# Optimization experiments

Hardware: AMD Instinct MI355X
Metric: run time of the kernel (lower is better)

The kernel has to match this reference:

```python
import jax, jax.numpy as jnp
import numpy as np

N_EMBD = 1024
N_HEAD = 16
LN_EPS = 1e-5


def layernorm(x, w, eps=LN_EPS):
    mu = jnp.mean(x, axis=-1, keepdims=True)
    var = jnp.mean(jnp.square(x - mu), axis=-1, keepdims=True)
    return (x - mu) * jax.lax.rsqrt(var + eps) * w


def setup_inputs() -> dict:
    key = jax.random.key(0)
    ks = jax.random.split(key, 6)
    B, T, C, F = 4, 2048, N_EMBD, 4 * N_EMBD
    s = 0.02
    return {
        "x": jax.random.normal(ks[0], (B, T, C), jnp.float32),
        "ln1_w": jnp.ones((C,), jnp.float32),
        "w_attn": jax.random.normal(ks[1], (C, 3 * C), jnp.float32) * s,
        "w_proj": jax.random.normal(ks[2], (C, C), jnp.float32) * s,
        "ln2_w": jnp.ones((C,), jnp.float32),
        "w_fc1": jax.random.normal(ks[3], (C, F), jnp.float32) * s,
        "b_fc1": jnp.zeros((F,), jnp.float32),
        "w_fc2": jax.random.normal(ks[4], (F, C), jnp.float32) * s,
        "b_fc2": jnp.zeros((C,), jnp.float32),
    }


def reference(x, ln1_w, w_attn, w_proj, ln2_w, w_fc1, b_fc1, w_fc2, b_fc2):
    B, T, C = x.shape
    H = N_HEAD
    D = C // H
    # --- attention sub-block (dropout = 0, eval mode) ---
    h = layernorm(x, ln1_w)
    qkv = h @ w_attn  # [B, T, 3C]
    q, k, v = jnp.split(qkv, 3, axis=-1)
    q = q.reshape(B, T, H, D)
    k = k.reshape(B, T, H, D)
    v = v.reshape(B, T, H, D)
    scale = 1.0 / np.sqrt(D).astype(np.float32)
    att = jnp.einsum("bqhd,bkhd->bhqk", q, k) * scale  # [B, H, T, T]
    causal = jnp.tril(jnp.ones((T, T), bool))
    att = jnp.where(causal, att, -jnp.inf)
    att = jax.nn.softmax(att, axis=-1)
    y = jnp.einsum("bhqk,bkhd->bqhd", att, v).reshape(B, T, C)
    x = x + y @ w_proj
    # --- MLP sub-block ---
    h = layernorm(x, ln2_w)
    h = jax.nn.relu(h @ w_fc1 + b_fc1)
    x = x + (h @ w_fc2 + b_fc2)
    return x
```

## Files before the change

### kernel.cpp

```cpp
#include <hip/hip_runtime.h>
#include <cstdint>


#define CDIM 1024
#define TSEQ 2048
#define NBATCH 4
#define NHEAD 16
#define HDIM 64
#define FDIM 4096

typedef unsigned short u16;
typedef __attribute__((ext_vector_type(8))) short s16x8;
typedef __attribute__((ext_vector_type(4))) float f32x4;

__device__ __forceinline__ u16 f2bu(float f) {
    uint32_t u = __builtin_bit_cast(uint32_t, f);
    uint32_t r = (u + 0x7FFFu + ((u >> 16) & 1u)) >> 16;
    return (u16)r;
}

__device__ __forceinline__ uint32_t cvtpk(float lo, float hi) {
    uint32_t r;
    asm("v_cvt_pk_bf16_f32 %0, %1, %2" : "=v"(r) : "v"(lo), "v"(hi));
    return r;
}

typedef __attribute__((address_space(3))) unsigned int lds_u32;
typedef __attribute__((address_space(1))) const unsigned int glb_u32;
__device__ __forceinline__ void gload_lds16(const void* g, void* l) {
    __builtin_amdgcn_global_load_lds((glb_u32*)g, (lds_u32*)l, 16, 0, 0);
}

__global__ __launch_bounds__(256) void twb_k(const float* __restrict__ in,
                                             u16* __restrict__ out, int K, int N) {
    __shared__ float tile[32][33];
    int n0 = blockIdx.x * 32, k0 = blockIdx.y * 32;
    int tx = threadIdx.x & 31, ty = threadIdx.x >> 5;
#pragma unroll
    for (int i = 0; i < 32; i += 8)
        tile[ty + i][tx] = in[(size_t)(k0 + ty + i) * N + n0 + tx];
    __syncthreads();
#pragma unroll
    for (int i = 0; i < 32; i += 8)
        out[(size_t)(n0 + ty + i) * K + k0 + tx] = f2bu(tile[tx][ty + i]);
}

__global__ __launch_bounds__(256) void ln_k(const float* __restrict__ x,
                                            const float* __restrict__ w,
                                            u16* __restrict__ out) {
    int row = blockIdx.x;
    int t = threadIdx.x;
    const float4* xr = (const float4*)(x + (size_t)row * CDIM);
    float4 v = xr[t];
    float s = v.x + v.y + v.z + v.w;
    float sq = v.x * v.x + v.y * v.y + v.z * v.z + v.w * v.w;
#pragma unroll
    for (int o = 32; o > 0; o >>= 1) { s += __shfl_xor(s, o); sq += __shfl_xor(sq, o); }
    __shared__ float ps[4], pq[4];
    int wid = t >> 6, lane = t & 63;
    if (lane == 0) { ps[wid] = s; pq[wid] = sq; }
    __syncthreads();
    s = ps[0] + ps[1] + ps[2] + ps[3];
    sq = pq[0] + pq[1] + pq[2] + pq[3];
    float mu = s * (1.0f / CDIM);
    float var = sq * (1.0f / CDIM) - mu * mu;
    float rstd = rsqrtf(var + 1e-5f);
    float4 wv = ((const float4*)w)[t];
    union { u16 h[4]; uint2 u; } pk;
    pk.h[0] = f2bu((v.x - mu) * rstd * wv.x);
    pk.h[1] = f2bu((v.y - mu) * rstd * wv.y);
    pk.h[2] = f2bu((v.z - mu) * rstd * wv.z);
    pk.h[3] = f2bu((v.w - mu) * rstd * wv.w);
    ((uint2*)(out + (size_t)row * CDIM))[t] = pk.u;
}

template <int EPI>
__global__ __launch_bounds__(256) void gemm_bt(const u16* __restrict__ A,
                                               const u16* __restrict__ Bt,
                                               void* __restrict__ Cout,
                                               u16* __restrict__ Vout,
                                               const float* __restrict__ bias,
                                               const float* __restrict__ res,
                                               int M, int N, int K) {
    __shared__ u16 Al[128 * 32];
    __shared__ u16 Bl[128 * 32];
    int tid = threadIdx.x;
    int lane = tid & 63, wid = tid >> 6;
    int wr = wid >> 1, wc = wid & 1;
    int lr = lane & 15, lk = lane >> 4;
    int m0 = blockIdx.y * 128, n0 = blockIdx.x * 128;

    f32x4 acc[4][4];
#pragma unroll
    for (int i = 0; i < 4; ++i)
#pragma unroll
        for (int j = 0; j < 4; ++j) acc[i][j] = (f32x4){0.f, 0.f, 0.f, 0.f};

    for (int k0 = 0; k0 < K; k0 += 32) {
        __syncthreads();
#pragma unroll
        for (int i = 0; i < 2; ++i) {
            int cb = (wid * 2 + i) * 64;
            int c = cb + lane;
            int r = c >> 2, kc = c & 3;
            gload_lds16(A + (size_t)(m0 + r) * K + k0 + kc * 8, Al + cb * 8);
            gload_lds16(Bt + (size_t)(n0 + r) * K + k0 + kc * 8, Bl + cb * 8);
        }
        __syncthreads();
        s16x8 af[4], bfr[4];
#pragma unroll
        for (int mi = 0; mi < 4; ++mi)
            af[mi] = *(const s16x8*)(Al + (wr * 64 + mi * 16 + lr) * 32 + lk * 8);
#pragma unroll
        for (int ni = 0; ni < 4; ++ni)
            bfr[ni] = *(const s16x8*)(Bl + (wc * 64 + ni * 16 + lr) * 32 + lk * 8);
#pragma unroll
        for (int mi = 0; mi < 4; ++mi)
#pragma unroll
            for (int ni = 0; ni < 4; ++ni)
                acc[mi][ni] = __builtin_amdgcn_mfma_f32_16x16x32_bf16(
                    af[mi], bfr[ni], acc[mi][ni], 0, 0, 0);
    }

#pragma unroll
    for (int mi = 0; mi < 4; ++mi) {
#pragma unroll
        for (int ni = 0; ni < 4; ++ni) {
            int col = n0 + wc * 64 + ni * 16 + lr;
#pragma unroll
            for (int r = 0; r < 4; ++r) {
                int row = m0 + wr * 64 + mi * 16 + lk * 4 + r;
                float v = acc[mi][ni][r];
                size_t idx = (size_t)row * N + col;
                if constexpr (EPI == 0) {
                    if (col < 2048) {
                        ((u16*)Cout)[idx] = f2bu(v);
                    } else {
                        int bb = row >> 11, tt = row & 2047, cc = col - 2048;
                        Vout[((size_t)(bb * 16 + (cc >> 6)) * 64 + (cc & 63)) * 2048 + tt] = f2bu(v);
                    }
                } else if constexpr (EPI == 1) {
                    ((float*)Cout)[idx] = res[idx] + v;
                } else if constexpr (EPI == 2) {
                    ((u16*)Cout)[idx] = f2bu(fmaxf(v + bias[col], 0.f));
                } else {
                    ((float*)Cout)[idx] = res[idx] + v + bias[col];
                }
            }
        }
    }
}

__global__ __launch_bounds__(256) void attn_k(const u16* __restrict__ qkv,
                                              const u16* __restrict__ vT,
                                              u16* __restrict__ y) {
    int pidx = blockIdx.x;
    int bh = blockIdx.y;
    int b = bh >> 4, h = bh & 15;
    int tid = threadIdx.x, lane = tid & 63, wid = tid >> 6;
    int lr = lane & 15, lk = lane >> 4;

    __shared__ u16 Kl[2][8192];
    __shared__ u16 Vl[2][8192];

    const u16* qkp = qkv + (size_t)(b * TSEQ) * 3072 + h * HDIM;
    const u16* kkp = qkp + CDIM;
    const u16* vtp = vT + (size_t)bh * HDIM * TSEQ;

    auto STAGE = [&](int buf, int kv0) {
#pragma unroll
        for (int c = 0; c < 4; ++c) {
            int s = c * 256 + wid * 64 + lane;
            int kr = s >> 3, kc = s & 7;
            int gkc = kc ^ (kr & 7);
            gload_lds16(kkp + (size_t)(kv0 + kr) * 3072 + gkc * 8,
                        &Kl[buf][(size_t)(c * 256 + wid * 64) * 8]);
            int vd = s >> 4, vc = s & 15;
            int gvc = (vc & 8) | ((vc ^ vd) & 7);
            gload_lds16(vtp + (size_t)vd * TSEQ + kv0 + gvc * 8,
                        &Vl[buf][(size_t)(c * 256 + wid * 64) * 8]);
        }
    };

    auto qtile = [&](int qt) {
        int qbase = qt * 128 + wid * 32;
        int qend = qbase + 31;
        s16x8 qf[2][2];
#pragma unroll
        for (int qs = 0; qs < 2; ++qs)
#pragma unroll
            for (int db = 0; db < 2; ++db)
                qf[qs][db] = *(const s16x8*)(qkp +
                    (size_t)(qbase + qs * 16 + lr) * 3072 + db * 32 + lk * 8);
        f32x4 acc[2][4];
#pragma unroll
        for (int qs = 0; qs < 2; ++qs)
#pragma unroll
            for (int ds = 0; ds < 4; ++ds) acc[qs][ds] = (f32x4){0.f, 0.f, 0.f, 0.f};
        float mrun[2] = {-1e30f, -1e30f};
        float lrun[2] = {0.f, 0.f};

        int nt = qt + 1;
        STAGE(0, 0);
        for (int t = 0; t < nt; ++t) {
            int cur = t & 1;
            int kv0 = t * 128;
            if (t + 1 < nt) {
                STAGE(cur ^ 1, (t + 1) * 128);
                asm volatile("s_waitcnt vmcnt(8)" ::: "memory");
            } else {
                asm volatile("s_waitcnt vmcnt(0)" ::: "memory");
            }
            __builtin_amdgcn_s_barrier();
            asm volatile("" ::: "memory");

            const u16* Kb = &Kl[cur][0];
            const u16* Vb = &Vl[cur][0];

            f32x4 st[8][2];
#pragma unroll
            for (int ks = 0; ks < 8; ++ks)
#pragma unroll
                for (int qs = 0; qs < 2; ++qs)
                    st[ks][qs] = (f32x4){-1e30f, -1e30f, -1e30f, -1e30f};
            __builtin_amdgcn_s_setprio(1);
#pragma unroll
            for (int ks = 0; ks < 8; ++ks) {
                if (kv0 + ks * 16 <= qend) {
                    s16x8 kf0 = *(const s16x8*)(Kb + (ks * 16 + lr) * 64 + ((lk ^ (lr & 7)) * 8));
                    s16x8 kf1 = *(const s16x8*)(Kb + (ks * 16 + lr) * 64 + (((4 + lk) ^ (lr & 7)) * 8));
#pragma unroll
                    for (int qs = 0; qs < 2; ++qs) {
                        f32x4 z = (f32x4){0.f, 0.f, 0.f, 0.f};
                        z = __builtin_amdgcn_mfma_f32_16x16x32_bf16(kf0, qf[qs][0], z, 0, 0, 0);
                        st[ks][qs] = __builtin_amdgcn_mfma_f32_16x16x32_bf16(kf1, qf[qs][1], z, 0, 0, 0);
                    }
                }
            }
            __builtin_amdgcn_s_setprio(0);

            if (kv0 + 127 > qbase) {
#pragma unroll
                for (int ks = 0; ks < 8; ++ks)
#pragma unroll
                    for (int qs = 0; qs < 2; ++qs)
#pragma unroll
                        for (int r = 0; r < 4; ++r) {
                            int k = kv0 + ks * 16 + lk * 4 + r;
                            int q = qbase + qs * 16 + lr;
                            if (k > q) st[ks][qs][r] = -1e30f;
                        }
            }

            uint32_t w[2][8][2];
#pragma unroll
            for (int qs = 0; qs < 2; ++qs) {
                float pmax = -1e30f;
#pragma unroll
                for (int ks = 0; ks < 8; ++ks) {
                    float a = fmaxf(fmaxf(st[ks][qs][0], st[ks][qs][1]),
                                    fmaxf(st[ks][qs][2], st[ks][qs][3]));
                    pmax = fmaxf(pmax, a);
                }
                pmax = fmaxf(pmax, __shfl_xor(pmax, 16));
                pmax = fmaxf(pmax, __shfl_xor(pmax, 32));
                float mnew = fmaxf(mrun[qs], pmax);
                float scale = __expf((mrun[qs] - mnew) * 0.125f);
                mrun[qs] = mnew;
                float psum = 0.f;
#pragma unroll
                for (int ks = 0; ks < 8; ++ks) {
#pragma unroll
                    for (int r = 0; r < 4; ++r) {
                        float pv = __expf((st[ks][qs][r] - mnew) * 0.125f);
                        st[ks][qs][r] = pv;
                        psum += pv;
                    }
                    w[qs][ks][0] = cvtpk(st[ks][qs][0], st[ks][qs][1]);
                    w[qs][ks][1] = cvtpk(st[ks][qs][2], st[ks][qs][3]);
                }
                psum += __shfl_xor(psum, 16);
                psum += __shfl_xor(psum, 32);
                lrun[qs] = lrun[qs] * scale + psum;
#pragma unroll
                for (int ds = 0; ds < 4; ++ds)
#pragma unroll
                    for (int r = 0; r < 4; ++r) acc[qs][ds][r] *= scale;
            }

            int A = lr + ((lane & 16) ? 32 : 0);
            bool hi = (lane & 32) != 0;
#pragma unroll
            for (int kh = 0; kh < 4; ++kh) {
                if (kv0 + kh * 32 <= qend) {
                    s16x8 vtf[4];
#pragma unroll
                    for (int ds = 0; ds < 4; ++ds) {
                        int ch = kh * 4 + lk;
                        int chs = (ch & 8) | ((ch ^ (lr & 7)) & 7);
                        vtf[ds] = *(const s16x8*)(Vb + (ds * 16 + lr) * 128 + chs * 8);
                    }
                    __builtin_amdgcn_s_setprio(1);
#pragma unroll
                    for (int qs = 0; qs < 2; ++qs) {
                        uint32_t p00 = (uint32_t)__shfl((int)w[qs][2 * kh][0], A);
                        uint32_t p01 = (uint32_t)__shfl((int)w[qs][2 * kh][1], A);
                        uint32_t p10 = (uint32_t)__shfl((int)w[qs][2 * kh + 1][0], A);
                        uint32_t p11 = (uint32_t)__shfl((int)w[qs][2 * kh + 1][1], A);
                        uint32_t q00 = (uint32_t)__shfl((int)w[qs][2 * kh][0], A + 16);
                        uint32_t q01 = (uint32_t)__shfl((int)w[qs][2 * kh][1], A + 16);
                        uint32_t q10 = (uint32_t)__shfl((int)w[qs][2 * kh + 1][0], A + 16);
                        uint32_t q11 = (uint32_t)__shfl((int)w[qs][2 * kh + 1][1], A + 16);
                        union { uint32_t u[4]; s16x8 v; } pf;
                        pf.u[0] = hi ? p10 : p00;
                        pf.u[1] = hi ? p11 : p01;
                        pf.u[2] = hi ? q10 : q00;
                        pf.u[3] = hi ? q11 : q01;
#pragma unroll
                        for (int ds = 0; ds < 4; ++ds)
                            acc[qs][ds] = __builtin_amdgcn_mfma_f32_16x16x32_bf16(
                                vtf[ds], pf.v, acc[qs][ds], 0, 0, 0);
                    }
                    __builtin_amdgcn_s_setprio(0);
                }
            }
            asm volatile("" ::: "memory");
            __builtin_amdgcn_s_barrier();
            asm volatile("" ::: "memory");
        }

        float rl[2] = {1.f / lrun[0], 1.f / lrun[1]};
#pragma unroll
        for (int qs = 0; qs < 2; ++qs) {
            int q = qbase + qs * 16 + lr;
            u16* yr = y + (size_t)(b * TSEQ + q) * CDIM + h * HDIM;
#pragma unroll
            for (int ds = 0; ds < 4; ++ds)
#pragma unroll
                for (int r = 0; r < 4; ++r)
                    yr[ds * 16 + lk * 4 + r] = f2bu(acc[qs][ds][r] * rl[qs]);
        }
    };

    qtile(pidx);
    qtile(15 - pidx);
}

extern "C" void kernel_launch(void* const* d_in, const int* in_sizes, int n_in,
                              void* d_out, int out_size, void* d_ws, size_t ws_size,
                              hipStream_t stream) {
    (void)in_sizes; (void)n_in; (void)out_size; (void)ws_size;
    const float* x      = (const float*)d_in[0];
    const float* ln1_w  = (const float*)d_in[1];
    const float* w_attn = (const float*)d_in[2];
    const float* w_proj = (const float*)d_in[3];
    const float* ln2_w  = (const float*)d_in[4];
    const float* w_fc1  = (const float*)d_in[5];
    const float* b_fc1  = (const float*)d_in[6];
    const float* w_fc2  = (const float*)d_in[7];
    const float* b_fc2  = (const float*)d_in[8];
    float* out = (float*)d_out;
    char* ws = (char*)d_ws;

    u16*   wT_attn = (u16*)(ws + 0);
    u16*   wT_proj = (u16*)(ws + 6291456);
    u16*   wT_fc1  = (u16*)(ws + 8388608);
    u16*   wT_fc2  = (u16*)(ws + 16777216);
    u16*   h       = (u16*)(ws + 25165824);
    u16*   qkvb    = (u16*)(ws + 41943040);
    u16*   yb      = (u16*)(ws + 92274688);
    float* x1      = (float*)(ws + 109051904);
    u16*   vTb     = (u16*)(ws + 109051904);
    u16*   h3      = (u16*)(ws + 41943040);

    twb_k<<<dim3(3072 / 32, 1024 / 32), 256, 0, stream>>>(w_attn, wT_attn, 1024, 3072);
    twb_k<<<dim3(1024 / 32, 1024 / 32), 256, 0, stream>>>(w_proj, wT_proj, 1024, 1024);
    twb_k<<<dim3(4096 / 32, 1024 / 32), 256, 0, stream>>>(w_fc1, wT_fc1, 1024, 4096);
    twb_k<<<dim3(1024 / 32, 4096 / 32), 256, 0, stream>>>(w_fc2, wT_fc2, 4096, 1024);

    ln_k<<<8192, 256, 0, stream>>>(x, ln1_w, h);
    gemm_bt<0><<<dim3(3072 / 128, 8192 / 128), 256, 0, stream>>>(h, wT_attn, qkvb, vTb, nullptr, nullptr, 8192, 3072, 1024);
    attn_k<<<dim3(8, NBATCH * NHEAD), 256, 0, stream>>>(qkvb, vTb, yb);
    gemm_bt<1><<<dim3(1024 / 128, 8192 / 128), 256, 0, stream>>>(yb, wT_proj, x1, nullptr, nullptr, x, 8192, 1024, 1024);
    ln_k<<<8192, 256, 0, stream>>>(x1, ln2_w, h);
    gemm_bt<2><<<dim3(4096 / 128, 8192 / 128), 256, 0, stream>>>(h, wT_fc1, h3, nullptr, b_fc1, nullptr, 8192, 4096, 1024);
    gemm_bt<3><<<dim3(1024 / 128, 8192 / 128), 256, 0, stream>>>(h3, wT_fc2, out, nullptr, b_fc2, x1, 8192, 1024, 4096);
}
```

Measured before the change: 620.9 us.

## Add 256x256 eight-wave pipelined GEMM for QKV and FC1, swizzle block order

Adds a new 512-thread GEMM kernel with 256x256 output tiles, a double-buffered LDS layout in 64-wide K slices, an XOR-swizzled LDS layout, and a barrier-paced schedule that interleaves LDS fragment loads, async global-to-LDS copies and MFMA blocks. It is used for the QKV and FC1 projections. The existing 128x128 GEMM gains an XCD-aware block-index swizzle. The larger tiles aim to raise arithmetic intensity and overlap loads with MFMA, at the cost of more registers and fewer concurrent blocks, and the prefetch wraps around to already-loaded tiles on the final iterations.

New measurement: 614.5 us. About the same (-1.0%).

```diff
diff --git a/kernel.cpp b/kernel.cpp
--- a/kernel.cpp
+++ b/kernel.cpp
@@ -30,6 +30,8 @@
 __device__ __forceinline__ void gload_lds16(const void* g, void* l) {
     __builtin_amdgcn_global_load_lds((glb_u32*)g, (lds_u32*)l, 16, 0, 0);
 }
+
+#define FENCE() asm volatile("" ::: "memory")
 
 __global__ __launch_bounds__(256) void twb_k(const float* __restrict__ in,
                                              u16* __restrict__ out, int K, int N) {
@@ -75,10 +77,125 @@
 }
 
 template <int EPI>
+__global__ __launch_bounds__(512, 2) void gemm8p(const u16* __restrict__ A,
+                                                 const u16* __restrict__ Bt,
+                                                 void* __restrict__ Cout,
+                                                 u16* __restrict__ Vout,
+                                                 const float* __restrict__ bias,
+                                                 int M, int N, int K) {
+    __shared__ __align__(16) u16 L[2][2][2][128][64];
+    const int tid = threadIdx.x, lane = tid & 63, wid = tid >> 6;
+    const int lr = lane & 15, lk = lane >> 4;
+    const int wr = wid >> 2, wcn = wid & 3;
+    const int nbx = gridDim.x;
+    const int nwg = nbx * gridDim.y;
+    const int bid = blockIdx.y * nbx + blockIdx.x;
+    const int swz = (bid & 7) * (nwg >> 3) + (bid >> 3);
+    const int m0 = (swz / nbx) * 256, n0 = (swz % nbx) * 256;
+    const int NT = K >> 6;
+
+    auto STG = [&](int kt, int part, int kh) {
+        const u16* src = part ? Bt : A;
+        const int base0 = part ? n0 : m0;
+        u16* dst = &L[kt & 1][part][kh][0][0];
+#pragma unroll
+        for (int i = 0; i < 2; ++i) {
+            int t = i * 512 + tid;
+            int r2 = t >> 3, se = t & 7;
+            int s = se ^ (r2 & 7);
+            int row = 2 * r2 + (s >> 2), c = s & 3;
+            gload_lds16(src + (size_t)(base0 + row) * K + kt * 64 + kh * 32 + c * 8,
+                        dst + (size_t)(i * 512 + wid * 64) * 8);
+        }
+    };
+
+    f32x4 acc[8][4];
+#pragma unroll
+    for (int i = 0; i < 8; ++i)
+#pragma unroll
+        for (int j = 0; j < 4; ++j) acc[i][j] = (f32x4){0.f, 0.f, 0.f, 0.f};
+
+    STG(0, 0, 0); STG(0, 1, 0); STG(0, 0, 1); STG(0, 1, 1);
+    STG(1, 0, 0); STG(1, 1, 0);
+    asm volatile("s_waitcnt vmcnt(8)" ::: "memory");
+    FENCE(); __builtin_amdgcn_s_barrier(); FENCE();
+
+    const int se = (((lr & 1) << 2) | lk) ^ (lr >> 1);
+    const int rA0 = wr * 64 + (lr >> 1);
+    const int rB0 = wcn * 32 + (lr >> 1);
+
+    s16x8 af[4], bf[4];
+
+#define LDA(kh, ch) \
+    { _Pragma("unroll") for (int q = 0; q < 4; ++q) \
+        af[q] = *(const s16x8*)&L[slot][0][kh][rA0 + (ch) * 32 + q * 8][se * 8]; }
+#define LDB(kh) \
+    { _Pragma("unroll") for (int q = 0; q < 4; ++q) \
+        bf[q] = *(const s16x8*)&L[slot][1][kh][rB0 + q * 8][se * 8]; }
+#define MM(ch) \
+    { __builtin_amdgcn_s_setprio(1); \
+      _Pragma("unroll") for (int qm = 0; qm < 4; ++qm) \
+      _Pragma("unroll") for (int ni = 0; ni < 4; ++ni) \
+        acc[(ch) * 4 + qm][ni] = __builtin_amdgcn_mfma_f32_16x16x32_bf16( \
+            af[qm], bf[ni], acc[(ch) * 4 + qm][ni], 0, 0, 0); \
+      __builtin_amdgcn_s_setprio(0); }
+#define BAR() { FENCE(); __builtin_amdgcn_s_barrier(); FENCE(); }
+#define CKPT() asm volatile("s_waitcnt vmcnt(8)" ::: "memory")
+
+    for (int j = 0; j < NT; ++j) {
+        const int slot = j & 1;
+        const int jn1 = (j + 1 < NT) ? j + 1 : j + 1 - NT;
+        const int jn2 = (j + 2 < NT) ? j + 2 : j + 2 - NT;
+        LDA(0, 0); LDB(0);
+        STG(jn1, 0, 1);
+        BAR(); MM(0); BAR();
+        LDA(0, 1);
+        STG(jn1, 1, 1);
+        CKPT();
+        BAR(); MM(1); BAR();
+        LDA(1, 0); LDB(1);
+        STG(jn2, 0, 0);
+        BAR(); MM(0); BAR();
+        LDA(1, 1);
+        STG(jn2, 1, 0);
+        CKPT();
+        BAR(); MM(1); BAR();
+    }
+#undef LDA
+#undef LDB
+#undef MM
+#undef BAR
+#undef CKPT
+
+#pragma unroll
+    for (int mi = 0; mi < 8; ++mi) {
+#pragma unroll
+        for (int ni = 0; ni < 4; ++ni) {
+            int col = n0 + wcn * 64 + ni * 16 + lr;
+#pragma unroll
+            for (int r = 0; r < 4; ++r) {
+                int row = m0 + wr * 128 + mi * 16 + lk * 4 + r;
+                float v = acc[mi][ni][r];
+                size_t idx = (size_t)row * N + col;
+                if constexpr (EPI == 0) {
+                    if (col < 2048) {
+                        ((u16*)Cout)[idx] = f2bu(v);
+                    } else {
+                        int bb = row >> 11, tt = row & 2047, cc = col - 2048;
+                        Vout[((size_t)(bb * 16 + (cc >> 6)) * 64 + (cc & 63)) * 2048 + tt] = f2bu(v);
+                    }
+                } else {
+                    ((u16*)Cout)[idx] = f2bu(fmaxf(v + bias[col], 0.f));
+                }
+            }
+        }
+    }
+}
+
+template <int EPI>
 __global__ __launch_bounds__(256) void gemm_bt(const u16* __restrict__ A,
                                                const u16* __restrict__ Bt,
                                                void* __restrict__ Cout,
-                                               u16* __restrict__ Vout,
                                                const float* __restrict__ bias,
                                                const float* __restrict__ res,
                                                int M, int N, int K) {
@@ -88,7 +205,11 @@
     int lane = tid & 63, wid = tid >> 6;
     int wr = wid >> 1, wc = wid & 1;
     int lr = lane & 15, lk = lane >> 4;
-    int m0 = blockIdx.y * 128, n0 = blockIdx.x * 128;
+    const int nbx = gridDim.x;
+    const int nwg = nbx * gridDim.y;
+    const int bid = blockIdx.y * nbx + blockIdx.x;
+    const int swz = (bid & 7) * (nwg >> 3) + (bid >> 3);
+    int m0 = (swz / nbx) * 128, n0 = (swz % nbx) * 128;
 
     f32x4 acc[4][4];
 #pragma unroll
@@ -132,17 +253,8 @@
                 int row = m0 + wr * 64 + mi * 16 + lk * 4 + r;
                 float v = acc[mi][ni][r];
                 size_t idx = (size_t)row * N + col;
-                if constexpr (EPI == 0) {
-                    if (col < 2048) {
-                        ((u16*)Cout)[idx] = f2bu(v);
-                    } else {
-                        int bb = row >> 11, tt = row & 2047, cc = col - 2048;
-                        Vout[((size_t)(bb * 16 + (cc >> 6)) * 64 + (cc & 63)) * 2048 + tt] = f2bu(v);
-                    }
-                } else if constexpr (EPI == 1) {
+                if constexpr (EPI == 1) {
                     ((float*)Cout)[idx] = res[idx] + v;
-                } else if constexpr (EPI == 2) {
-                    ((u16*)Cout)[idx] = f2bu(fmaxf(v + bias[col], 0.f));
                 } else {
                     ((float*)Cout)[idx] = res[idx] + v + bias[col];
                 }
@@ -212,7 +324,7 @@
                 asm volatile("s_waitcnt vmcnt(0)" ::: "memory");
             }
             __builtin_amdgcn_s_barrier();
-            asm volatile("" ::: "memory");
+            FENCE();
 
             const u16* Kb = &Kl[cur][0];
             const u16* Vb = &Vl[cur][0];
@@ -324,9 +436,9 @@
                     __builtin_amdgcn_s_setprio(0);
                 }
             }
-            asm volatile("" ::: "memory");
+            FENCE();
             __builtin_amdgcn_s_barrier();
-            asm volatile("" ::: "memory");
+            FENCE();
         }
 
         float rl[2] = {1.f / lrun[0], 1.f / lrun[1]};
@@ -379,10 +491,10 @@
     twb_k<<<dim3(1024 / 32, 4096 / 32), 256, 0, stream>>>(w_fc2, wT_fc2, 4096, 1024);
 
     ln_k<<<8192, 256, 0, stream>>>(x, ln1_w, h);
-    gemm_bt<0><<<dim3(3072 / 128, 8192 / 128), 256, 0, stream>>>(h, wT_attn, qkvb, vTb, nullptr, nullptr, 8192, 3072, 1024);
+    gemm8p<0><<<dim3(3072 / 256, 8192 / 256), 512, 0, stream>>>(h, wT_attn, qkvb, vTb, nullptr, 8192, 3072, 1024);
     attn_k<<<dim3(8, NBATCH * NHEAD), 256, 0, stream>>>(qkvb, vTb, yb);
-    gemm_bt<1><<<dim3(1024 / 128, 8192 / 128), 256, 0, stream>>>(yb, wT_proj, x1, nullptr, nullptr, x, 8192, 1024, 1024);
+    gemm_bt<1><<<dim3(1024 / 128, 8192 / 128), 256, 0, stream>>>(yb, wT_proj, x1, nullptr, x, 8192, 1024, 1024);
     ln_k<<<8192, 256, 0, stream>>>(x1, ln2_w, h);
-    gemm_bt<2><<<dim3(4096 / 128, 8192 / 128), 256, 0, stream>>>(h, wT_fc1, h3, nullptr, b_fc1, nullptr, 8192, 4096, 1024);
-    gemm_bt<3><<<dim3(1024 / 128, 8192 / 128), 256, 0, stream>>>(h3, wT_fc2, out, nullptr, b_fc2, x1, 8192, 1024, 4096);
-}
+    gemm8p<2><<<dim3(4096 / 256, 8192 / 256), 512, 0, stream>>>(h, wT_fc1, h3, nullptr, b_fc1, 8192, 4096, 1024);
+    gemm_bt<3><<<dim3(1024 / 128, 8192 / 128), 256, 0, stream>>>(h3, wT_fc2, out, b_fc2, x1, 8192, 1024, 4096);
+}
```
